# Optimization experiments

Hardware: AMD Instinct MI355X
Metric: run time of the kernel (lower is better)

Reference implementation:

```python
import jax, jax.numpy as jnp
import numpy as np

SELF_DIM = 64
NB_DIM = 64
HID = 256
K = 16  # num_use_neighbor_obs


def _ff(x, w1, b1, w2, b2):
    # FeedForward: Linear -> GELU (exact erf, torch nn.GELU default) -> Linear
    return jax.nn.gelu(x @ w1 + b1, approximate=False) @ w2 + b2


def setup_inputs() -> dict:
    key = jax.random.key(0)
    ks = jax.random.split(key, 9)
    B = 8192
    s = 0.02
    return {
        "self_obs": jax.random.normal(ks[0], (B, SELF_DIM), jnp.float32),
        "obs": jax.random.normal(ks[1], (B, SELF_DIM + K * NB_DIM), jnp.float32),
        "We1": jax.random.normal(ks[2], (SELF_DIM + NB_DIM, 4 * (SELF_DIM + NB_DIM)), jnp.float32) * s,
        "be1": jnp.zeros((4 * (SELF_DIM + NB_DIM),), jnp.float32),
        "We2": jax.random.normal(ks[3], (4 * (SELF_DIM + NB_DIM), HID), jnp.float32) * s,
        "be2": jnp.zeros((HID,), jnp.float32),
        "Wv1": jax.random.normal(ks[4], (HID, 4 * HID), jnp.float32) * s,
        "bv1": jnp.zeros((4 * HID,), jnp.float32),
        "Wv2": jax.random.normal(ks[5], (4 * HID, HID), jnp.float32) * s,
        "bv2": jnp.zeros((HID,), jnp.float32),
        "Wa1": jax.random.normal(ks[6], (2 * HID, 8 * HID), jnp.float32) * s,
        "ba1": jnp.zeros((8 * HID,), jnp.float32),
        "Wa2": jax.random.normal(ks[7], (8 * HID, 1), jnp.float32) * s,
        "ba2": jnp.zeros((1,), jnp.float32),
        "all_neighbor_obs_size": K * NB_DIM,
        "batch_size": 8192,
    }


def reference(self_obs, obs, We1, be1, We2, be2, Wv1, bv1, Wv2, bv2,
              Wa1, ba1, Wa2, ba2, all_neighbor_obs_size, batch_size):
    # neighbor obs: (B, K*nd) -> (B*K, nd), batch-major row order
    obs_neighbors = obs[:, SELF_DIM:SELF_DIM + all_neighbor_obs_size].reshape(-1, NB_DIM)
    # torch .repeat(K, 1): tiles the whole batch K times -> neighbor-major order
    self_obs_repeat = jnp.tile(self_obs, (K, 1))  # (K*B, self_dim)
    mlp_input = jnp.concatenate([self_obs_repeat, obs_neighbors], axis=1)
    neighbor_embeddings = _ff(mlp_input, We1, be1, We2, be2)          # (B*K, H)
    neighbor_values = _ff(neighbor_embeddings, Wv1, bv1, Wv2, bv2)    # (B*K, H)
    emb_mean = neighbor_embeddings.reshape(batch_size, -1, HID).mean(axis=1)  # (B, H)
    emb_mean_repeat = jnp.tile(emb_mean, (K, 1))                      # (K*B, H)
    attn_in = jnp.concatenate([neighbor_embeddings, emb_mean_repeat], axis=1)
    attn_logits = _ff(attn_in, Wa1, ba1, Wa2, ba2).reshape(batch_size, -1)  # (B, K)
    attn = jax.nn.softmax(attn_logits, axis=1).reshape(-1, 1)         # (B*K, 1)
    final = (attn * neighbor_values).reshape(batch_size, -1, HID).sum(axis=1)
    return final
```

## Files before the change

### kernel.cpp

```cpp
#include <hip/hip_runtime.h>
#include <hip/hip_bf16.h>

#define B_SZ 8192
#define KNB 16
#define BK 131072
#define ED 256

typedef __attribute__((ext_vector_type(8))) short short8v;
typedef __attribute__((ext_vector_type(4))) float floatx4;

static __device__ __forceinline__ unsigned short f2bf(float f) {
  unsigned int u = __float_as_uint(f);
  u = (u + 0x7FFFu + ((u >> 16) & 1u)) >> 16;
  return (unsigned short)u;
}
static __device__ __forceinline__ float bf2f(unsigned short u) {
  return __uint_as_float(((unsigned int)u) << 16);
}
static __device__ __forceinline__ float gelu_erf(float x) {
  return 0.5f * x * (1.0f + erff(x * 0.70710678118654752f));
}
static __device__ __forceinline__ float gelu_poly(float x) {
  float t = x * x;
  float p = fmaf(t, fmaf(t, fmaf(t, fmaf(t, 2.8935185185e-4f, -2.9761904762e-3f),
                                 2.5e-2f), -1.6666666667e-1f), 1.0f);
  return 0.5f * x * fmaf(0.79788456080286536f * x, p, 1.0f);
}

#define MFMA(a, b, c) __builtin_amdgcn_mfma_f32_16x16x32_bf16((a), (b), (c), 0, 0, 0)

static __device__ __forceinline__ void gll16(const void* g, void* l) {
  __builtin_amdgcn_global_load_lds(
      (const __attribute__((address_space(1))) unsigned int*)g,
      (__attribute__((address_space(3))) unsigned int*)l, 16, 0, 0);
}

__global__ void wt_kernel(const float* __restrict__ W, unsigned short* __restrict__ WT,
                          int K, int N) {
  int idx = blockIdx.x * 256 + threadIdx.x;
  if (idx >= K * N) return;
  int n = idx / K, k = idx - n * K;
  WT[idx] = f2bf(W[(size_t)k * N + n]);
}

__global__ void wf_kernel(const float* __restrict__ W, unsigned short* __restrict__ WF,
                          int ldw) {
  int idx = blockIdx.x * 256 + threadIdx.x;
  int f = idx >> 9;
  int w = idx & 511;
  int ln = w >> 3, i = w & 7;
  int ctile = f >> 3, kk = f & 7;
  int col = ctile * 16 + (ln & 15);
  int k = kk * 32 + (ln >> 4) * 8 + i;
  WF[idx] = f2bf(W[(size_t)k * ldw + col]);
}

__global__ __launch_bounds__(256) void k1_kernel(
    const float* __restrict__ self_obs, const float* __restrict__ obs,
    const unsigned short* __restrict__ We1T, const float* __restrict__ be1,
    const unsigned short* __restrict__ We2T, const float* __restrict__ be2,
    unsigned short* __restrict__ E, unsigned short* __restrict__ M) {
  __shared__ unsigned short Xt[64][136];
  __shared__ unsigned short Ht[64][136];
  const int tid = threadIdx.x;
  const int wave = tid >> 6, lane = tid & 63, g = lane >> 4, r = lane & 15;
  const int row0 = blockIdx.x * 64;

#pragma unroll
  for (int p = 0; p < 8; ++p) {
    int e4 = (p * 256 + tid) * 4;
    int i = e4 >> 7, c = e4 & 127;
    int gi = row0 + i;
    const float* src;
    if (c < 64) src = self_obs + (size_t)(gi & (B_SZ - 1)) * 64 + c;
    else        src = obs + (size_t)(gi >> 4) * 1088 + 64 + (gi & 15) * 64 + (c - 64);
    float4 v = *(const float4*)src;
    ushort4 w;
    w.x = f2bf(v.x); w.y = f2bf(v.y); w.z = f2bf(v.z); w.w = f2bf(v.w);
    *(ushort4*)&Xt[i][c] = w;
  }
  __syncthreads();

  floatx4 eacc[4][4];
#pragma unroll
  for (int a = 0; a < 4; ++a)
#pragma unroll
    for (int c2 = 0; c2 < 4; ++c2) eacc[a][c2] = (floatx4)0.0f;

  for (int chunk = 0; chunk < 4; ++chunk) {
    const int hbase = chunk * 128;
    floatx4 hacc[2][4];
#pragma unroll
    for (int a = 0; a < 2; ++a)
#pragma unroll
      for (int c2 = 0; c2 < 4; ++c2) hacc[a][c2] = (floatx4)0.0f;

#pragma unroll
    for (int kk = 0; kk < 4; ++kk) {
      short8v afr[4];
#pragma unroll
      for (int rt = 0; rt < 4; ++rt)
        afr[rt] = *(const short8v*)&Xt[rt * 16 + r][kk * 32 + g * 8];
#pragma unroll
      for (int ctl = 0; ctl < 2; ++ctl) {
        int col = hbase + wave * 32 + ctl * 16 + r;
        short8v bfr = *(const short8v*)&We1T[(size_t)col * 128 + kk * 32 + g * 8];
#pragma unroll
        for (int rt = 0; rt < 4; ++rt) hacc[ctl][rt] = MFMA(afr[rt], bfr, hacc[ctl][rt]);
      }
    }
#pragma unroll
    for (int ctl = 0; ctl < 2; ++ctl) {
      int col = hbase + wave * 32 + ctl * 16 + r;
      float bias = be1[col];
#pragma unroll
      for (int rt = 0; rt < 4; ++rt)
#pragma unroll
        for (int q = 0; q < 4; ++q) {
          float h = gelu_erf(hacc[ctl][rt][q] + bias);
          Ht[rt * 16 + g * 4 + q][wave * 32 + ctl * 16 + r] = f2bf(h);
        }
    }
    __syncthreads();
#pragma unroll
    for (int kk = 0; kk < 4; ++kk) {
      short8v afr[4];
#pragma unroll
      for (int rt = 0; rt < 4; ++rt)
        afr[rt] = *(const short8v*)&Ht[rt * 16 + r][kk * 32 + g * 8];
#pragma unroll
      for (int ct = 0; ct < 4; ++ct) {
        int col = wave * 64 + ct * 16 + r;
        short8v bfr = *(const short8v*)&We2T[(size_t)col * 512 + hbase + kk * 32 + g * 8];
#pragma unroll
        for (int rt = 0; rt < 4; ++rt) eacc[rt][ct] = MFMA(afr[rt], bfr, eacc[rt][ct]);
      }
    }
    __syncthreads();
  }

#pragma unroll
  for (int ct = 0; ct < 4; ++ct) {
    int col = wave * 64 + ct * 16 + r;
    float bias = be2[col];
#pragma unroll
    for (int rt = 0; rt < 4; ++rt) {
      float msum = 0.f;
#pragma unroll
      for (int q = 0; q < 4; ++q) {
        float e = eacc[rt][ct][q] + bias;
        int row = rt * 16 + g * 4 + q;
        E[(size_t)(row0 + row) * ED + col] = f2bf(e);
        msum += e;
      }
      msum += __shfl_xor(msum, 16);
      msum += __shfl_xor(msum, 32);
      if (g == 0) {
        int b = (row0 >> 4) + rt;
        M[(size_t)b * ED + col] = f2bf(msum * 0.0625f);
      }
    }
  }
}

__global__ __launch_bounds__(512) void k2_mv(
    const unsigned short* __restrict__ M, const unsigned short* __restrict__ Wa1T,
    const float* __restrict__ ba1, unsigned short* __restrict__ MV) {
  __shared__ unsigned short Abuf[128 * 64];
  __shared__ unsigned short Bbuf[256 * 64];
  const int tid = threadIdx.x;
  const int wave = tid >> 6, lane = tid & 63, g = lane >> 4, r = lane & 15;
  const int wr = wave >> 2, wc = wave & 3;
  const int row0 = blockIdx.y * 128;
  const int col0 = blockIdx.x * 256;
  const int sr = lane >> 3, sc = lane & 7;
  const int swz = ((sc ^ sr) << 4);

  floatx4 acc[4][4];
#pragma unroll
  for (int a = 0; a < 4; ++a)
#pragma unroll
    for (int c2 = 0; c2 < 4; ++c2) acc[a][c2] = (floatx4)0.0f;

  for (int t = 0; t < 4; ++t) {
#pragma unroll
    for (int j = 0; j < 2; ++j) {
      int rowA = j * 64 + wave * 8 + sr;
      const char* src = (const char*)M + ((size_t)(row0 + rowA)) * 512 + t * 128 + swz;
      gll16(src, (char*)Abuf + (j * 512 + wave * 64) * 16);
    }
#pragma unroll
    for (int j = 0; j < 4; ++j) {
      int colB = j * 64 + wave * 8 + sr;
      const char* src = (const char*)Wa1T + ((size_t)(col0 + colB)) * 1024 + 512
                        + t * 128 + swz;
      gll16(src, (char*)Bbuf + (j * 512 + wave * 64) * 16);
    }
    __syncthreads();
#pragma unroll
    for (int kk = 0; kk < 2; ++kk) {
      const int off = (kk * 64 + g * 16) ^ ((r & 7) << 4);
      short8v afr[4], bfr[4];
#pragma unroll
      for (int rt = 0; rt < 4; ++rt)
        afr[rt] = *(const short8v*)((const char*)Abuf + (wr * 64 + rt * 16 + r) * 128 + off);
#pragma unroll
      for (int ct = 0; ct < 4; ++ct)
        bfr[ct] = *(const short8v*)((const char*)Bbuf + (wc * 64 + ct * 16 + r) * 128 + off);
#pragma unroll
      for (int rt = 0; rt < 4; ++rt)
#pragma unroll
        for (int ct = 0; ct < 4; ++ct) acc[rt][ct] = MFMA(afr[rt], bfr[ct], acc[rt][ct]);
    }
    __syncthreads();
  }

#pragma unroll
  for (int ct = 0; ct < 4; ++ct) {
    int col = col0 + wc * 64 + ct * 16 + r;
    float b1 = ba1[col];
#pragma unroll
    for (int rt = 0; rt < 4; ++rt)
#pragma unroll
      for (int q = 0; q < 4; ++q)
        MV[(size_t)(row0 + wr * 64 + rt * 16 + g * 4 + q) * 2048 + col] =
            f2bf(acc[rt][ct][q] + b1);
  }
}

__global__ __launch_bounds__(512, 4) void k3_fused(
    const unsigned short* __restrict__ E, const unsigned short* __restrict__ MV,
    const unsigned short* __restrict__ Wa1F, const float* __restrict__ Wa2,
    const unsigned short* __restrict__ Wv1F, const float* __restrict__ bv1,
    unsigned short* __restrict__ G) {
  __shared__ char Bq[65536];
  const int tid = threadIdx.x;
  const int wave = tid >> 6, lane = tid & 63, g = lane >> 4, r = lane & 15;
  const int bid = blockIdx.x;
  const int knb0 = wave * 2;
  const int jr = bid * 16 + r;

  short8v er0[8], er1[8];
  {
    const unsigned short* e0 = E + ((size_t)knb0 * 8192 + jr) * 256 + g * 8;
    const unsigned short* e1 = e0 + (size_t)8192 * 256;
#pragma unroll
    for (int kk = 0; kk < 8; ++kk) {
      er0[kk] = *(const short8v*)(e0 + kk * 32);
      er1[kk] = *(const short8v*)(e1 + kk * 32);
    }
  }

  auto STAGE = [&](const unsigned short* WF, int c) {
    char* dst = Bq + (c & 3) * 16384 + wave * 2048;
    const char* src = (const char*)WF + (size_t)c * 16384 + wave * 2048 + lane * 16;
    gll16(src, dst);
    gll16(src + 1024, dst + 1024);
  };

  const unsigned short* mvp = MV + (size_t)jr * 2048;
  float lgp0 = 0.f, lgp1 = 0.f;

  auto CHUNK_A = [&](int c) {
    ushort4 mq[2];
    float4 w2[2];
#pragma unroll
    for (int ct = 0; ct < 2; ++ct) {
      mq[ct] = *(const ushort4*)(mvp + c * 32 + ct * 16 + g * 4);
      w2[ct] = *(const float4*)&Wa2[c * 32 + ct * 16 + g * 4];
    }
    floatx4 acc0[2], acc1[2];
    acc0[0] = (floatx4)0.0f; acc0[1] = (floatx4)0.0f;
    acc1[0] = (floatx4)0.0f; acc1[1] = (floatx4)0.0f;
    const char* bufb = Bq + (c & 3) * 16384;
#pragma unroll
    for (int kk = 0; kk < 8; ++kk) {
#pragma unroll
      for (int ct = 0; ct < 2; ++ct) {
        short8v a = *(const short8v*)(bufb + (ct * 8 + kk) * 1024 + lane * 16);
        acc0[ct] = MFMA(a, er0[kk], acc0[ct]);
        acc1[ct] = MFMA(a, er1[kk], acc1[ct]);
      }
    }
#pragma unroll
    for (int ct = 0; ct < 2; ++ct) {
      const float* wp = (const float*)&w2[ct];
      const unsigned short* mp = (const unsigned short*)&mq[ct];
#pragma unroll
      for (int q = 0; q < 4; ++q) {
        float mvv = bf2f(mp[q]);
        lgp0 = fmaf(gelu_poly(acc0[ct][q] + mvv), wp[q], lgp0);
        lgp1 = fmaf(gelu_poly(acc1[ct][q] + mvv), wp[q], lgp1);
      }
    }
  };

  float aw0 = 0.f, aw1 = 0.f;

  auto CHUNK_B = [&](int c) {
    float4 b1[2];
#pragma unroll
    for (int ct = 0; ct < 2; ++ct)
      b1[ct] = *(const float4*)&bv1[c * 32 + ct * 16 + g * 4];
    floatx4 acc0[2], acc1[2];
    acc0[0] = (floatx4)0.0f; acc0[1] = (floatx4)0.0f;
    acc1[0] = (floatx4)0.0f; acc1[1] = (floatx4)0.0f;
    const char* bufb = Bq + (c & 3) * 16384;
#pragma unroll
    for (int kk = 0; kk < 8; ++kk) {
#pragma unroll
      for (int ct = 0; ct < 2; ++ct) {
        short8v a = *(const short8v*)(bufb + (ct * 8 + kk) * 1024 + lane * 16);
        acc0[ct] = MFMA(a, er0[kk], acc0[ct]);
        acc1[ct] = MFMA(a, er1[kk], acc1[ct]);
      }
    }
#pragma unroll
    for (int ct = 0; ct < 2; ++ct) {
      const float* bp = (const float*)&b1[ct];
      ushort4 p0, p1;
      unsigned short* pp0 = (unsigned short*)&p0;
      unsigned short* pp1 = (unsigned short*)&p1;
#pragma unroll
      for (int q = 0; q < 4; ++q) {
        float v0 = gelu_poly(acc0[ct][q] + bp[q]) * aw0;
        float v1 = gelu_poly(acc1[ct][q] + bp[q]) * aw1;
        v0 += __shfl_xor(v0, 1); v0 += __shfl_xor(v0, 2);
        v0 += __shfl_xor(v0, 4); v0 += __shfl_xor(v0, 8);
        v1 += __shfl_xor(v1, 1); v1 += __shfl_xor(v1, 2);
        v1 += __shfl_xor(v1, 4); v1 += __shfl_xor(v1, 8);
        pp0[q] = f2bf(v0);
        pp1[q] = f2bf(v1);
      }
      if (r == 0) {
        size_t b0 = (size_t)(knb0 * 512 + bid);
        *(ushort4*)&G[b0 * 1024 + c * 32 + ct * 16 + g * 4] = p0;
        *(ushort4*)&G[(b0 + 512) * 1024 + c * 32 + ct * 16 + g * 4] = p1;
      }
    }
  };

  STAGE(Wa1F, 0); STAGE(Wa1F, 1);
  __syncthreads();
  for (int gi = 0; gi < 31; ++gi) {
    const int c = gi * 2;
    STAGE(Wa1F, c + 2); STAGE(Wa1F, c + 3);
    CHUNK_A(c); CHUNK_A(c + 1);
    __syncthreads();
  }
  STAGE(Wv1F, 0); STAGE(Wv1F, 1);
  CHUNK_A(62); CHUNK_A(63);
  __syncthreads();

  lgp0 += __shfl_xor(lgp0, 16); lgp0 += __shfl_xor(lgp0, 32);
  lgp1 += __shfl_xor(lgp1, 16); lgp1 += __shfl_xor(lgp1, 32);
  float m0 = lgp0, m1 = lgp1;
  m0 = fmaxf(m0, __shfl_xor(m0, 1)); m0 = fmaxf(m0, __shfl_xor(m0, 2));
  m0 = fmaxf(m0, __shfl_xor(m0, 4)); m0 = fmaxf(m0, __shfl_xor(m0, 8));
  m1 = fmaxf(m1, __shfl_xor(m1, 1)); m1 = fmaxf(m1, __shfl_xor(m1, 2));
  m1 = fmaxf(m1, __shfl_xor(m1, 4)); m1 = fmaxf(m1, __shfl_xor(m1, 8));
  float e0 = expf(lgp0 - m0), e1 = expf(lgp1 - m1);
  float s0 = e0, s1 = e1;
  s0 += __shfl_xor(s0, 1); s0 += __shfl_xor(s0, 2);
  s0 += __shfl_xor(s0, 4); s0 += __shfl_xor(s0, 8);
  s1 += __shfl_xor(s1, 1); s1 += __shfl_xor(s1, 2);
  s1 += __shfl_xor(s1, 4); s1 += __shfl_xor(s1, 8);
  aw0 = e0 / s0;
  aw1 = e1 / s1;

  for (int gi = 0; gi < 16; ++gi) {
    const int c = gi * 2;
    if (gi < 15) { STAGE(Wv1F, c + 2); STAGE(Wv1F, c + 3); }
    CHUNK_B(c); CHUNK_B(c + 1);
    __syncthreads();
  }
}

__global__ __launch_bounds__(256) void k5b_gemm(
    const unsigned short* __restrict__ G, const unsigned short* __restrict__ Wv2T,
    const float* __restrict__ bv2, float* __restrict__ out) {
  __shared__ unsigned short Abuf[64 * 64];
  __shared__ unsigned short Bbuf[128 * 64];
  const int tid = threadIdx.x;
  const int wave = tid >> 6, lane = tid & 63, g = lane >> 4, r = lane & 15;
  const int wr = wave >> 1, wc = wave & 1;
  const int col0 = blockIdx.x * 128;
  const int row0 = blockIdx.y * 64;
  const int sr = lane >> 3, sc = lane & 7;
  const int swz = ((sc ^ sr) << 4);

  floatx4 acc[2][4];
#pragma unroll
  for (int a = 0; a < 2; ++a)
#pragma unroll
    for (int c2 = 0; c2 < 4; ++c2) acc[a][c2] = (floatx4)0.0f;

  for (int t = 0; t < 16; ++t) {
#pragma unroll
    for (int j = 0; j < 2; ++j) {
      int rowA = j * 32 + wave * 8 + sr;
      const char* src = (const char*)G + ((size_t)(row0 + rowA)) * 2048 + t * 128 + swz;
      gll16(src, (char*)Abuf + (j * 256 + wave * 64) * 16);
    }
#pragma unroll
    for (int j = 0; j < 4; ++j) {
      int colB = j * 32 + wave * 8 + sr;
      const char* src = (const char*)Wv2T + ((size_t)(col0 + colB)) * 2048 + t * 128 + swz;
      gll16(src, (char*)Bbuf + (j * 256 + wave * 64) * 16);
    }
    __syncthreads();
#pragma unroll
    for (int kk = 0; kk < 2; ++kk) {
      const int off = (kk * 64 + g * 16) ^ ((r & 7) << 4);
      short8v afr[2], bfr[4];
#pragma unroll
      for (int rt = 0; rt < 2; ++rt)
        afr[rt] = *(const short8v*)((const char*)Abuf + (wr * 32 + rt * 16 + r) * 128 + off);
#pragma unroll
      for (int ct = 0; ct < 4; ++ct)
        bfr[ct] = *(const short8v*)((const char*)Bbuf + (wc * 64 + ct * 16 + r) * 128 + off);
#pragma unroll
      for (int rt = 0; rt < 2; ++rt)
#pragma unroll
        for (int ct = 0; ct < 4; ++ct) acc[rt][ct] = MFMA(afr[rt], bfr[ct], acc[rt][ct]);
    }
    __syncthreads();
  }

#pragma unroll
  for (int ct = 0; ct < 4; ++ct) {
    int col = col0 + wc * 64 + ct * 16 + r;
    float b = bv2[col];
#pragma unroll
    for (int rt = 0; rt < 2; ++rt)
#pragma unroll
      for (int q = 0; q < 4; ++q)
        out[(size_t)(row0 + wr * 32 + rt * 16 + g * 4 + q) * ED + col] =
            acc[rt][ct][q] + b;
  }
}

extern "C" void kernel_launch(void* const* d_in, const int* in_sizes, int n_in,
                              void* d_out, int out_size, void* d_ws, size_t ws_size,
                              hipStream_t stream) {
  const float* self_obs = (const float*)d_in[0];
  const float* obs = (const float*)d_in[1];
  const float* We1 = (const float*)d_in[2];
  const float* be1 = (const float*)d_in[3];
  const float* We2 = (const float*)d_in[4];
  const float* be2 = (const float*)d_in[5];
  const float* Wv1 = (const float*)d_in[6];
  const float* bv1 = (const float*)d_in[7];
  const float* Wv2 = (const float*)d_in[8];
  const float* bv2 = (const float*)d_in[9];
  const float* Wa1 = (const float*)d_in[10];
  const float* ba1 = (const float*)d_in[11];
  const float* Wa2 = (const float*)d_in[12];
  const float* ba2 = (const float*)d_in[13];
  float* out = (float*)d_out;
  (void)ba2;

  char* ws = (char*)d_ws;
  size_t off = 0;
  auto alloc = [&](size_t bytes) {
    char* p = ws + off;
    off += (bytes + 255) & ~(size_t)255;
    return p;
  };
  unsigned short* E    = (unsigned short*)alloc((size_t)BK * ED * 2);
  unsigned short* M    = (unsigned short*)alloc((size_t)B_SZ * ED * 2);
  unsigned short* MV   = (unsigned short*)alloc((size_t)B_SZ * 2048 * 2);
  unsigned short* G    = (unsigned short*)alloc((size_t)B_SZ * 1024 * 2);
  unsigned short* We1T = (unsigned short*)alloc(128 * 512 * 2);
  unsigned short* We2T = (unsigned short*)alloc(512 * 256 * 2);
  unsigned short* Wv2T = (unsigned short*)alloc(1024 * 256 * 2);
  unsigned short* Wa1T = (unsigned short*)alloc(512 * 2048 * 2);
  unsigned short* Wa1F = (unsigned short*)alloc(2048 * 256 * 2);
  unsigned short* Wv1F = (unsigned short*)alloc(1024 * 256 * 2);

  wt_kernel<<<(128 * 512 + 255) / 256, 256, 0, stream>>>(We1, We1T, 128, 512);
  wt_kernel<<<(512 * 256 + 255) / 256, 256, 0, stream>>>(We2, We2T, 512, 256);
  wt_kernel<<<(1024 * 256 + 255) / 256, 256, 0, stream>>>(Wv2, Wv2T, 1024, 256);
  wt_kernel<<<(512 * 2048 + 255) / 256, 256, 0, stream>>>(Wa1, Wa1T, 512, 2048);
  wf_kernel<<<2048, 256, 0, stream>>>(Wa1, Wa1F, 2048);
  wf_kernel<<<1024, 256, 0, stream>>>(Wv1, Wv1F, 1024);

  k1_kernel<<<BK / 64, 256, 0, stream>>>(self_obs, obs, We1T, be1, We2T, be2, E, M);
  k2_mv<<<dim3(8, 64), 512, 0, stream>>>(M, Wa1T, ba1, MV);
  k3_fused<<<B_SZ / 16, 512, 0, stream>>>(E, MV, Wa1F, Wa2, Wv1F, bv1, G);
  k5b_gemm<<<dim3(2, 128), 256, 0, stream>>>(G, Wv2T, bv2, out);
}
```

Before: 492.4 us.

## Transpose MFMA operands in fused attention kernel and store MV column-major

Swaps the MFMA operand order in k3_fused so each lane's accumulator holds four batch rows for a single output column rather than four columns for one row. To match, k2 now writes MV transposed, so each lane reads a contiguous ushort4 of four rows, and it stores four packed values per write. The value-weighting step now accumulates the attention-weighted sum over rows in registers with two cross-group shuffles, replacing the previous four-level shuffle per element, and writes per-column results. The costs are strided scalar loads of Wa2 and bv1, a transposed MVT read pattern with an 8192-element stride between columns, and narrower 2-byte G stores.

```diff
diff --git a/kernel.cpp b/kernel.cpp
--- a/kernel.cpp
+++ b/kernel.cpp
@@ -165,7 +165,7 @@
 
 __global__ __launch_bounds__(512) void k2_mv(
     const unsigned short* __restrict__ M, const unsigned short* __restrict__ Wa1T,
-    const float* __restrict__ ba1, unsigned short* __restrict__ MV) {
+    const float* __restrict__ ba1, unsigned short* __restrict__ MVT) {
   __shared__ unsigned short Abuf[128 * 64];
   __shared__ unsigned short Bbuf[256 * 64];
   const int tid = threadIdx.x;
@@ -220,16 +220,19 @@
     int col = col0 + wc * 64 + ct * 16 + r;
     float b1 = ba1[col];
 #pragma unroll
-    for (int rt = 0; rt < 4; ++rt)
-#pragma unroll
-      for (int q = 0; q < 4; ++q)
-        MV[(size_t)(row0 + wr * 64 + rt * 16 + g * 4 + q) * 2048 + col] =
-            f2bf(acc[rt][ct][q] + b1);
+    for (int rt = 0; rt < 4; ++rt) {
+      ushort4 st;
+      st.x = f2bf(acc[rt][ct][0] + b1);
+      st.y = f2bf(acc[rt][ct][1] + b1);
+      st.z = f2bf(acc[rt][ct][2] + b1);
+      st.w = f2bf(acc[rt][ct][3] + b1);
+      *(ushort4*)&MVT[(size_t)col * 8192 + row0 + wr * 64 + rt * 16 + g * 4] = st;
+    }
   }
 }
 
 __global__ __launch_bounds__(512, 4) void k3_fused(
-    const unsigned short* __restrict__ E, const unsigned short* __restrict__ MV,
+    const unsigned short* __restrict__ E, const unsigned short* __restrict__ MVT,
     const unsigned short* __restrict__ Wa1F, const float* __restrict__ Wa2,
     const unsigned short* __restrict__ Wv1F, const float* __restrict__ bv1,
     unsigned short* __restrict__ G) {
@@ -238,11 +241,10 @@
   const int wave = tid >> 6, lane = tid & 63, g = lane >> 4, r = lane & 15;
   const int bid = blockIdx.x;
   const int knb0 = wave * 2;
-  const int jr = bid * 16 + r;
 
   short8v er0[8], er1[8];
   {
-    const unsigned short* e0 = E + ((size_t)knb0 * 8192 + jr) * 256 + g * 8;
+    const unsigned short* e0 = E + ((size_t)knb0 * 8192 + bid * 16 + r) * 256 + g * 8;
     const unsigned short* e1 = e0 + (size_t)8192 * 256;
 #pragma unroll
     for (int kk = 0; kk < 8; ++kk) {
@@ -251,127 +253,130 @@
     }
   }
 
-  auto STAGE = [&](const unsigned short* WF, int c) {
-    char* dst = Bq + (c & 3) * 16384 + wave * 2048;
-    const char* src = (const char*)WF + (size_t)c * 16384 + wave * 2048 + lane * 16;
+  auto STAGE = [&](int t) {
+    const char* src = (t < 64 ? (const char*)Wa1F + (size_t)t * 16384
+                              : (const char*)Wv1F + (size_t)(t - 64) * 16384)
+                      + wave * 2048 + lane * 16;
+    char* dst = Bq + (t & 3) * 16384 + wave * 2048;
     gll16(src, dst);
     gll16(src + 1024, dst + 1024);
   };
 
-  const unsigned short* mvp = MV + (size_t)jr * 2048;
-  float lgp0 = 0.f, lgp1 = 0.f;
-
-  auto CHUNK_A = [&](int c) {
-    ushort4 mq[2];
-    float4 w2[2];
+  float lgp0[4] = {0.f, 0.f, 0.f, 0.f}, lgp1[4] = {0.f, 0.f, 0.f, 0.f};
+  const size_t mrow = (size_t)bid * 16 + g * 4;
+
+  auto CHUNK_A = [&](int t) {
+    const int c0 = t * 32;
+    float w2[2];
+    ushort4 mv[2];
 #pragma unroll
     for (int ct = 0; ct < 2; ++ct) {
-      mq[ct] = *(const ushort4*)(mvp + c * 32 + ct * 16 + g * 4);
-      w2[ct] = *(const float4*)&Wa2[c * 32 + ct * 16 + g * 4];
+      w2[ct] = Wa2[c0 + ct * 16 + r];
+      mv[ct] = *(const ushort4*)&MVT[(size_t)(c0 + ct * 16 + r) * 8192 + mrow];
     }
     floatx4 acc0[2], acc1[2];
     acc0[0] = (floatx4)0.0f; acc0[1] = (floatx4)0.0f;
     acc1[0] = (floatx4)0.0f; acc1[1] = (floatx4)0.0f;
-    const char* bufb = Bq + (c & 3) * 16384;
+    const char* bufb = Bq + (t & 3) * 16384;
 #pragma unroll
     for (int kk = 0; kk < 8; ++kk) {
 #pragma unroll
       for (int ct = 0; ct < 2; ++ct) {
         short8v a = *(const short8v*)(bufb + (ct * 8 + kk) * 1024 + lane * 16);
-        acc0[ct] = MFMA(a, er0[kk], acc0[ct]);
-        acc1[ct] = MFMA(a, er1[kk], acc1[ct]);
+        acc0[ct] = MFMA(er0[kk], a, acc0[ct]);
+        acc1[ct] = MFMA(er1[kk], a, acc1[ct]);
       }
     }
 #pragma unroll
     for (int ct = 0; ct < 2; ++ct) {
-      const float* wp = (const float*)&w2[ct];
-      const unsigned short* mp = (const unsigned short*)&mq[ct];
+      const unsigned short* mp = (const unsigned short*)&mv[ct];
 #pragma unroll
       for (int q = 0; q < 4; ++q) {
         float mvv = bf2f(mp[q]);
-        lgp0 = fmaf(gelu_poly(acc0[ct][q] + mvv), wp[q], lgp0);
-        lgp1 = fmaf(gelu_poly(acc1[ct][q] + mvv), wp[q], lgp1);
+        lgp0[q] = fmaf(gelu_poly(acc0[ct][q] + mvv), w2[ct], lgp0[q]);
+        lgp1[q] = fmaf(gelu_poly(acc1[ct][q] + mvv), w2[ct], lgp1[q]);
       }
     }
   };
 
-  float aw0 = 0.f, aw1 = 0.f;
-
-  auto CHUNK_B = [&](int c) {
-    float4 b1[2];
-#pragma unroll
-    for (int ct = 0; ct < 2; ++ct)
-      b1[ct] = *(const float4*)&bv1[c * 32 + ct * 16 + g * 4];
+  float aw0[4], aw1[4];
+
+  auto CHUNK_B = [&](int t) {
+    const int c0 = (t - 64) * 32;
+    float b1[2];
+#pragma unroll
+    for (int ct = 0; ct < 2; ++ct) b1[ct] = bv1[c0 + ct * 16 + r];
     floatx4 acc0[2], acc1[2];
     acc0[0] = (floatx4)0.0f; acc0[1] = (floatx4)0.0f;
     acc1[0] = (floatx4)0.0f; acc1[1] = (floatx4)0.0f;
-    const char* bufb = Bq + (c & 3) * 16384;
+    const char* bufb = Bq + (t & 3) * 16384;
 #pragma unroll
     for (int kk = 0; kk < 8; ++kk) {
 #pragma unroll
       for (int ct = 0; ct < 2; ++ct) {
         short8v a = *(const short8v*)(bufb + (ct * 8 + kk) * 1024 + lane * 16);
-        acc0[ct] = MFMA(a, er0[kk], acc0[ct]);
-        acc1[ct] = MFMA(a, er1[kk], acc1[ct]);
-      }
-    }
+        acc0[ct] = MFMA(er0[kk], a, acc0[ct]);
+        acc1[ct] = MFMA(er1[kk], a, acc1[ct]);
+      }
+    }
+    float ps0[2], ps1[2];
+    ps0[0] = 0.f; ps0[1] = 0.f; ps1[0] = 0.f; ps1[1] = 0.f;
+#pragma unroll
+    for (int ct = 0; ct < 2; ++ct)
+#pragma unroll
+      for (int q = 0; q < 4; ++q) {
+        ps0[ct] = fmaf(gelu_poly(acc0[ct][q] + b1[ct]), aw0[q], ps0[ct]);
+        ps1[ct] = fmaf(gelu_poly(acc1[ct][q] + b1[ct]), aw1[q], ps1[ct]);
+      }
 #pragma unroll
     for (int ct = 0; ct < 2; ++ct) {
-      const float* bp = (const float*)&b1[ct];
-      ushort4 p0, p1;
-      unsigned short* pp0 = (unsigned short*)&p0;
-      unsigned short* pp1 = (unsigned short*)&p1;
-#pragma unroll
-      for (int q = 0; q < 4; ++q) {
-        float v0 = gelu_poly(acc0[ct][q] + bp[q]) * aw0;
-        float v1 = gelu_poly(acc1[ct][q] + bp[q]) * aw1;
-        v0 += __shfl_xor(v0, 1); v0 += __shfl_xor(v0, 2);
-        v0 += __shfl_xor(v0, 4); v0 += __shfl_xor(v0, 8);
-        v1 += __shfl_xor(v1, 1); v1 += __shfl_xor(v1, 2);
-        v1 += __shfl_xor(v1, 4); v1 += __shfl_xor(v1, 8);
-        pp0[q] = f2bf(v0);
-        pp1[q] = f2bf(v1);
-      }
-      if (r == 0) {
-        size_t b0 = (size_t)(knb0 * 512 + bid);
-        *(ushort4*)&G[b0 * 1024 + c * 32 + ct * 16 + g * 4] = p0;
-        *(ushort4*)&G[(b0 + 512) * 1024 + c * 32 + ct * 16 + g * 4] = p1;
+      ps0[ct] += __shfl_xor(ps0[ct], 16); ps0[ct] += __shfl_xor(ps0[ct], 32);
+      ps1[ct] += __shfl_xor(ps1[ct], 16); ps1[ct] += __shfl_xor(ps1[ct], 32);
+    }
+    if (g == 0) {
+      size_t b0 = (size_t)(knb0 * 512 + bid);
+#pragma unroll
+      for (int ct = 0; ct < 2; ++ct) {
+        G[b0 * 1024 + c0 + ct * 16 + r] = f2bf(ps0[ct]);
+        G[(b0 + 512) * 1024 + c0 + ct * 16 + r] = f2bf(ps1[ct]);
       }
     }
   };
 
-  STAGE(Wa1F, 0); STAGE(Wa1F, 1);
+  STAGE(0); STAGE(1);
   __syncthreads();
-  for (int gi = 0; gi < 31; ++gi) {
-    const int c = gi * 2;
-    STAGE(Wa1F, c + 2); STAGE(Wa1F, c + 3);
-    CHUNK_A(c); CHUNK_A(c + 1);
-    __syncthreads();
-  }
-  STAGE(Wv1F, 0); STAGE(Wv1F, 1);
-  CHUNK_A(62); CHUNK_A(63);
-  __syncthreads();
-
-  lgp0 += __shfl_xor(lgp0, 16); lgp0 += __shfl_xor(lgp0, 32);
-  lgp1 += __shfl_xor(lgp1, 16); lgp1 += __shfl_xor(lgp1, 32);
-  float m0 = lgp0, m1 = lgp1;
-  m0 = fmaxf(m0, __shfl_xor(m0, 1)); m0 = fmaxf(m0, __shfl_xor(m0, 2));
-  m0 = fmaxf(m0, __shfl_xor(m0, 4)); m0 = fmaxf(m0, __shfl_xor(m0, 8));
-  m1 = fmaxf(m1, __shfl_xor(m1, 1)); m1 = fmaxf(m1, __shfl_xor(m1, 2));
-  m1 = fmaxf(m1, __shfl_xor(m1, 4)); m1 = fmaxf(m1, __shfl_xor(m1, 8));
-  float e0 = expf(lgp0 - m0), e1 = expf(lgp1 - m1);
-  float s0 = e0, s1 = e1;
-  s0 += __shfl_xor(s0, 1); s0 += __shfl_xor(s0, 2);
-  s0 += __shfl_xor(s0, 4); s0 += __shfl_xor(s0, 8);
-  s1 += __shfl_xor(s1, 1); s1 += __shfl_xor(s1, 2);
-  s1 += __shfl_xor(s1, 4); s1 += __shfl_xor(s1, 8);
-  aw0 = e0 / s0;
-  aw1 = e1 / s1;
-
-  for (int gi = 0; gi < 16; ++gi) {
-    const int c = gi * 2;
-    if (gi < 15) { STAGE(Wv1F, c + 2); STAGE(Wv1F, c + 3); }
-    CHUNK_B(c); CHUNK_B(c + 1);
+  for (int t0 = 0; t0 < 64; t0 += 2) {
+    STAGE(t0 + 2); STAGE(t0 + 3);
+    CHUNK_A(t0); CHUNK_A(t0 + 1);
+    __syncthreads();
+  }
+
+#pragma unroll
+  for (int q = 0; q < 4; ++q) {
+    lgp0[q] += __shfl_xor(lgp0[q], 1); lgp0[q] += __shfl_xor(lgp0[q], 2);
+    lgp0[q] += __shfl_xor(lgp0[q], 4); lgp0[q] += __shfl_xor(lgp0[q], 8);
+    lgp1[q] += __shfl_xor(lgp1[q], 1); lgp1[q] += __shfl_xor(lgp1[q], 2);
+    lgp1[q] += __shfl_xor(lgp1[q], 4); lgp1[q] += __shfl_xor(lgp1[q], 8);
+  }
+  float m0 = fmaxf(fmaxf(lgp0[0], lgp0[1]), fmaxf(lgp0[2], lgp0[3]));
+  float m1 = fmaxf(fmaxf(lgp1[0], lgp1[1]), fmaxf(lgp1[2], lgp1[3]));
+  m0 = fmaxf(m0, __shfl_xor(m0, 16)); m0 = fmaxf(m0, __shfl_xor(m0, 32));
+  m1 = fmaxf(m1, __shfl_xor(m1, 16)); m1 = fmaxf(m1, __shfl_xor(m1, 32));
+  float s0 = 0.f, s1 = 0.f;
+#pragma unroll
+  for (int q = 0; q < 4; ++q) {
+    aw0[q] = expf(lgp0[q] - m0); s0 += aw0[q];
+    aw1[q] = expf(lgp1[q] - m1); s1 += aw1[q];
+  }
+  s0 += __shfl_xor(s0, 16); s0 += __shfl_xor(s0, 32);
+  s1 += __shfl_xor(s1, 16); s1 += __shfl_xor(s1, 32);
+  float is0 = 1.f / s0, is1 = 1.f / s1;
+#pragma unroll
+  for (int q = 0; q < 4; ++q) { aw0[q] *= is0; aw1[q] *= is1; }
+
+  for (int t0 = 64; t0 < 96; t0 += 2) {
+    if (t0 + 2 < 96) { STAGE(t0 + 2); STAGE(t0 + 3); }
+    CHUNK_B(t0); CHUNK_B(t0 + 1);
     __syncthreads();
   }
 }
@@ -469,7 +474,7 @@
   };
   unsigned short* E    = (unsigned short*)alloc((size_t)BK * ED * 2);
   unsigned short* M    = (unsigned short*)alloc((size_t)B_SZ * ED * 2);
-  unsigned short* MV   = (unsigned short*)alloc((size_t)B_SZ * 2048 * 2);
+  unsigned short* MVT  = (unsigned short*)alloc((size_t)B_SZ * 2048 * 2);
   unsigned short* G    = (unsigned short*)alloc((size_t)B_SZ * 1024 * 2);
   unsigned short* We1T = (unsigned short*)alloc(128 * 512 * 2);
   unsigned short* We2T = (unsigned short*)alloc(512 * 256 * 2);
@@ -486,7 +491,7 @@
   wf_kernel<<<1024, 256, 0, stream>>>(Wv1, Wv1F, 1024);
 
   k1_kernel<<<BK / 64, 256, 0, stream>>>(self_obs, obs, We1T, be1, We2T, be2, E, M);
-  k2_mv<<<dim3(8, 64), 512, 0, stream>>>(M, Wa1T, ba1, MV);
-  k3_fused<<<B_SZ / 16, 512, 0, stream>>>(E, MV, Wa1F, Wa2, Wv1F, bv1, G);
+  k2_mv<<<dim3(8, 64), 512, 0, stream>>>(M, Wa1T, ba1, MVT);
+  k3_fused<<<B_SZ / 16, 512, 0, stream>>>(E, MVT, Wa1F, Wa2, Wv1F, bv1, G);
   k5b_gemm<<<dim3(2, 128), 256, 0, stream>>>(G, Wv2T, bv2, out);
 }
```

Result: slower. 585.3 us (+18.9%).
